# Optimization experiments

Hardware: AMD Instinct MI355X
Metric: run time of the kernel (lower is better)

The kernel has to match this reference:

```python
import jax, jax.numpy as jnp
import numpy as np
from jax import lax

SOS_TOKEN = 0
PAD_LEN = 30  # tokenizer.pad_len -> number of greedy decode steps


def _gru_cell(x, h, w_ih, w_hh, b_ih, b_hh):
    # PyTorch GRU cell math. x,h: [B,H]; w_*: [3H,H]; b_*: [3H]
    gi = x @ w_ih.T + b_ih
    gh = h @ w_hh.T + b_hh
    i_r, i_z, i_n = jnp.split(gi, 3, axis=-1)
    h_r, h_z, h_n = jnp.split(gh, 3, axis=-1)
    r = jax.nn.sigmoid(i_r + h_r)
    z = jax.nn.sigmoid(i_z + h_z)
    n = jnp.tanh(i_n + r * h_n)
    return (1.0 - z) * n + z * h


def _sm_encode(sm_hidden, conv_w, conv_b, enc_w, enc_b):
    # sm_hidden: [B, L, C] -> conv over time with C input channels
    x = jnp.transpose(sm_hidden, (0, 2, 1))  # [B, C, L]
    conv = lax.conv_general_dilated(
        x, conv_w, window_strides=(1,), padding='VALID',
        dimension_numbers=('NCH', 'OIH', 'NCH'))  # [B, O, L-k+1]
    conv = jax.nn.relu(conv + conv_b[None, :, None])
    pooled = jnp.max(conv, axis=-1)  # [B, O]
    return jax.nn.relu(pooled @ enc_w.T + enc_b)  # [B, H]


def reference(sm_hidden, embedding, w_ih, w_hh, b_ih, b_hh,
              w_out, b_out, conv_w, conv_b, enc_w, enc_b):
    B = sm_hidden.shape[0]
    h0 = _sm_encode(sm_hidden, conv_w, conv_b, enc_w, enc_b)  # [B, H]

    # The original re-runs the GRU over the whole (append-only) prefix each
    # iteration; since the GRU is deterministic this equals incremental
    # single-step updates, which we do here.
    def step(carry, _):
        h, tok = carry
        emb = embedding[tok]                      # [B, H]
        h_new = _gru_cell(emb, h, w_ih, w_hh, b_ih, b_hh)
        logits = h_new @ w_out.T + b_out          # [B, V]
        tok_new = jnp.argmax(logits, axis=-1)     # greedy topk(1)
        return (h_new, tok_new), (h_new, tok_new)

    tok0 = jnp.full((B,), SOS_TOKEN, dtype=jnp.int32)
    (h_last, _), (hiddens, toks) = lax.scan(step, (h0, tok0), None, length=PAD_LEN)

    decoder_output = jax.nn.log_softmax(h_last @ w_out.T + b_out, axis=1)  # [B, V]
    decoder_hidden = hiddens  # [PAD_LEN, B, H] == rnn_out of final _base_forward
    decoded_indices = jnp.concatenate([tok0[None, :], toks], axis=0)  # [PAD_LEN+1, B]
    return decoder_output, decoder_hidden, decoded_indices


def setup_inputs() -> dict:
    key = jax.random.key(0)
    ks = jax.random.split(key, 12)
    B, L, C = 512, 120, 128
    H, V, O, K = 1024, 512, 32, 10
    s = 1.0 / np.sqrt(H)
    return {
        'sm_hidden': jax.random.normal(ks[0], (B, L, C), jnp.float32),
        'embedding': jax.random.normal(ks[1], (V, H), jnp.float32),
        'w_ih': jax.random.uniform(ks[2], (3 * H, H), jnp.float32, -s, s),
        'w_hh': jax.random.uniform(ks[3], (3 * H, H), jnp.float32, -s, s),
        'b_ih': jax.random.uniform(ks[4], (3 * H,), jnp.float32, -s, s),
        'b_hh': jax.random.uniform(ks[5], (3 * H,), jnp.float32, -s, s),
        'w_out': jax.random.uniform(ks[6], (V, H), jnp.float32, -s, s),
        'b_out': jax.random.uniform(ks[7], (V,), jnp.float32, -s, s),
        'conv_w': jax.random.normal(ks[8], (O, C, K), jnp.float32) * 0.05,
        'conv_b': jax.random.normal(ks[9], (O,), jnp.float32) * 0.05,
        'enc_w': jax.random.uniform(ks[10], (H, O), jnp.float32, -s, s),
        'enc_b': jax.random.uniform(ks[11], (H,), jnp.float32, -s, s),
    }
```

## Files before the change

kernel.cpp:

```cpp
#include <hip/hip_runtime.h>
#include <hip/hip_bf16.h>
#include <math.h>

#define Bsz 512
#define Hd 1024
#define Vd 512
#define Cc 128
#define Ll 120
#define Kk 10
#define Oo 32
#define NSTEP 30

typedef __attribute__((ext_vector_type(8))) short bf16x8;
typedef __attribute__((ext_vector_type(4))) float f32x4;
typedef unsigned short ushort;
typedef unsigned long long u64;

#define BARLDS() asm volatile("s_waitcnt lgkmcnt(0)\n\ts_barrier" ::: "memory")

static __device__ __forceinline__ float sigm(float x) { return 1.f / (1.f + expf(-x)); }
static __device__ __forceinline__ ushort f2bf(float x) {
    __hip_bfloat16 h = __float2bfloat16(x);
    return *(ushort*)&h;
}
static __device__ __forceinline__ float bf2f(ushort u) {
    __hip_bfloat16 h; *(ushort*)&h = u;
    return __bfloat162float(h);
}
static __device__ __forceinline__ unsigned monofy(float f) {
    unsigned u = __float_as_uint(f);
    return (u & 0x80000000u) ? ~u : (u | 0x80000000u);
}

__global__ void k_packall(const float* __restrict__ wih, ushort* __restrict__ wihH, ushort* __restrict__ wihL,
                          const float* __restrict__ whh, ushort* __restrict__ whhH, ushort* __restrict__ whhL,
                          const float* __restrict__ wout, ushort* __restrict__ woutH, ushort* __restrict__ woutL,
                          const float* __restrict__ emb, ushort* __restrict__ embH, ushort* __restrict__ embL) {
    int gidx = blockIdx.x * 256 + threadIdx.x;
    const float* W;
    ushort *hi, *lo;
    int idx;
    if (gidx < 3145728)      { W = wih;  hi = wihH;  lo = wihL;  idx = gidx; }
    else if (gidx < 6291456) { W = whh;  hi = whhH;  lo = whhL;  idx = gidx - 3145728; }
    else if (gidx < 6815744) { W = wout; hi = woutH; lo = woutL; idx = gidx - 6291456; }
    else if (gidx < 7340032) { W = emb;  hi = embH;  lo = embL;  idx = gidx - 6815744; }
    else return;
    int jj = idx & 7, l = (idx >> 3) & 63, c = (idx >> 9) & 31, nf = idx >> 14;
    int n = nf * 16 + (l & 15);
    int k = c * 32 + ((l >> 4) << 3) + jj;
    float v = W[(size_t)n * 1024 + k];
    ushort h = f2bf(v);
    hi[idx] = h;
    lo[idx] = f2bf(v - bf2f(h));
}

__global__ void k_packconv(const float* __restrict__ cw, ushort* __restrict__ hi,
                           ushort* __restrict__ lo) {
    int idx = blockIdx.x * 256 + threadIdx.x;
    if (idx >= 2 * 40 * 64 * 8) return;
    int jj = idx & 7, l = (idx >> 3) & 63, ch = (idx >> 9) % 40, nf = idx / (40 * 512);
    int o = nf * 16 + (l & 15);
    int k = ch * 32 + ((l >> 4) << 3) + jj;
    int kc = k >> 7, c = k & 127;
    float v = cw[(o * Cc + c) * Kk + kc];
    ushort h = f2bf(v);
    hi[idx] = h;
    lo[idx] = f2bf(v - bf2f(h));
}

__global__ __launch_bounds__(512) void k_convmfma(const float* __restrict__ sm,
                                                  const ushort* __restrict__ wH,
                                                  const ushort* __restrict__ wL,
                                                  const float* __restrict__ cb,
                                                  const float* __restrict__ ew,
                                                  const float* __restrict__ eb,
                                                  float* __restrict__ h0,
                                                  ushort* __restrict__ ApHi,
                                                  ushort* __restrict__ ApLo) {
    __shared__ ushort hiS[2][137 * 128];
    __shared__ ushort loS[2][137 * 128];
    __shared__ float sred[8][2][2][16];
    __shared__ float ps[2][Oo];
    int b0 = blockIdx.x * 2, tid = threadIdx.x, wid = tid >> 6, l = tid & 63;

    for (int i = tid; i < 3840; i += 512) {
        int s = i >= 1920;
        int local = i - s * 1920;
        int row = local >> 4, col0 = (local & 15) * 8;
        const float* smb = sm + (size_t)(b0 + s) * (Ll * Cc);
        float4 fa = *(const float4*)(smb + row * Cc + col0);
        float4 fb = *(const float4*)(smb + row * Cc + col0 + 4);
        float vv[8] = {fa.x, fa.y, fa.z, fa.w, fb.x, fb.y, fb.z, fb.w};
        ushort h8[8], l8[8];
#pragma unroll
        for (int q = 0; q < 8; ++q) {
            ushort h = f2bf(vv[q]);
            h8[q] = h;
            l8[q] = f2bf(vv[q] - bf2f(h));
        }
        int o = ((row << 8) + (col0 << 1)) ^ ((row & 7) << 4);
        *(bf16x8*)((char*)hiS[s] + o) = *(bf16x8*)h8;
        *(bf16x8*)((char*)loS[s] + o) = *(bf16x8*)l8;
    }
    __syncthreads();

    f32x4 acc[2][2];
#pragma unroll
    for (int s = 0; s < 2; ++s)
#pragma unroll
        for (int j = 0; j < 2; ++j) acc[s][j] = (f32x4)0.f;

    bf16x8 aH0[2], aL0[2], bH0[2], bL0[2];
    bf16x8 aH1[2], aL1[2], bH1[2], bL1[2];

#define CLD(AH, AL, BH, BL, ch)                                                        \
    {                                                                                  \
        int row = wid * 16 + (l & 15) + ((ch) >> 2);                                   \
        int o = ((row << 8) + ((((ch) & 3) * 32 + ((l >> 4) << 3)) << 1))              \
                ^ ((row & 7) << 4);                                                    \
        _Pragma("unroll") for (int s = 0; s < 2; ++s) {                                \
            AH[s] = *(const bf16x8*)((const char*)hiS[s] + o);                         \
            AL[s] = *(const bf16x8*)((const char*)loS[s] + o);                         \
        }                                                                              \
        _Pragma("unroll") for (int nf = 0; nf < 2; ++nf) {                             \
            int boff = ((nf * 40 + (ch)) * 64 + l) * 8;                                \
            BH[nf] = *(const bf16x8*)(wH + boff);                                      \
            BL[nf] = *(const bf16x8*)(wL + boff);                                      \
        }                                                                              \
    }
#define CST(AH, AL, BH, BL)                                                            \
    {                                                                                  \
        _Pragma("unroll") for (int s = 0; s < 2; ++s)                                  \
            _Pragma("unroll") for (int nf = 0; nf < 2; ++nf) {                         \
                acc[s][nf] = __builtin_amdgcn_mfma_f32_16x16x32_bf16(AH[s], BH[nf], acc[s][nf], 0, 0, 0); \
                acc[s][nf] = __builtin_amdgcn_mfma_f32_16x16x32_bf16(AH[s], BL[nf], acc[s][nf], 0, 0, 0); \
                acc[s][nf] = __builtin_amdgcn_mfma_f32_16x16x32_bf16(AL[s], BH[nf], acc[s][nf], 0, 0, 0); \
            }                                                                          \
    }

    CLD(aH0, aL0, bH0, bL0, 0)
#pragma unroll
    for (int ch = 0; ch < 40; ch += 2) {
        CLD(aH1, aL1, bH1, bL1, ch + 1)
        CST(aH0, aL0, bH0, bL0)
        if (ch + 2 < 40) CLD(aH0, aL0, bH0, bL0, ch + 2)
        CST(aH1, aL1, bH1, bL1)
    }
#undef CLD
#undef CST

    float mx[2][2] = {{-1e38f, -1e38f}, {-1e38f, -1e38f}};
    {
        int tb = wid * 16 + ((l >> 4) << 2);
#pragma unroll
        for (int q = 0; q < 4; ++q) {
            if (tb + q <= 110) {
#pragma unroll
                for (int s = 0; s < 2; ++s) {
                    mx[s][0] = fmaxf(mx[s][0], acc[s][0][q]);
                    mx[s][1] = fmaxf(mx[s][1], acc[s][1][q]);
                }
            }
        }
    }
#pragma unroll
    for (int sh = 16; sh < 64; sh <<= 1) {
#pragma unroll
        for (int s = 0; s < 2; ++s) {
            mx[s][0] = fmaxf(mx[s][0], __shfl_xor(mx[s][0], sh));
            mx[s][1] = fmaxf(mx[s][1], __shfl_xor(mx[s][1], sh));
        }
    }
    if (l < 16) {
#pragma unroll
        for (int s = 0; s < 2; ++s) {
            sred[wid][s][0][l] = mx[s][0];
            sred[wid][s][1][l] = mx[s][1];
        }
    }
    __syncthreads();
    if (tid < 64) {
        int s = tid >> 5, o = tid & 31;
        float m = sred[0][s][o >> 4][o & 15];
#pragma unroll
        for (int w = 1; w < 8; ++w) m = fmaxf(m, sred[w][s][o >> 4][o & 15]);
        ps[s][o] = fmaxf(m + cb[o], 0.f);
    }
    __syncthreads();
    for (int j = tid; j < Hd; j += 512) {
        const float4* e4 = (const float4*)(ew + (size_t)j * Oo);
        float4 w0 = e4[0], w1 = e4[1], w2 = e4[2], w3 = e4[3];
        float4 w4 = e4[4], w5 = e4[5], w6 = e4[6], w7 = e4[7];
        float ebj = eb[j];
        int c = j >> 5, sub = (j >> 3) & 3, jj = j & 7;
#pragma unroll
        for (int s = 0; s < 2; ++s) {
            int b = b0 + s;
            const float* p = ps[s];
            float a = ebj;
            a += p[0] * w0.x + p[1] * w0.y + p[2] * w0.z + p[3] * w0.w;
            a += p[4] * w1.x + p[5] * w1.y + p[6] * w1.z + p[7] * w1.w;
            a += p[8] * w2.x + p[9] * w2.y + p[10] * w2.z + p[11] * w2.w;
            a += p[12] * w3.x + p[13] * w3.y + p[14] * w3.z + p[15] * w3.w;
            a += p[16] * w4.x + p[17] * w4.y + p[18] * w4.z + p[19] * w4.w;
            a += p[20] * w5.x + p[21] * w5.y + p[22] * w5.z + p[23] * w5.w;
            a += p[24] * w6.x + p[25] * w6.y + p[26] * w6.z + p[27] * w6.w;
            a += p[28] * w7.x + p[29] * w7.y + p[30] * w7.z + p[31] * w7.w;
            a = fmaxf(a, 0.f);
            h0[(size_t)b * Hd + j] = a;
            ushort hb = f2bf(a);
            ushort lb = f2bf(a - bf2f(hb));
            int amf = b >> 4;
            int lane_r = (b & 15) + (sub << 4);
            int flat = ((amf * 32 + c) * 64 + lane_r) * 8 + jj;
            ApHi[flat] = hb;
            ApLo[flat] = lb;
        }
    }
}

template <int EPI>
__global__ __launch_bounds__(512, 2) void k_rnn(const ushort* __restrict__ Ah,
                                                const ushort* __restrict__ Al,
                                                const ushort* __restrict__ Bh,
                                                const ushort* __restrict__ Bl,
                                                const float* __restrict__ bias,
                                                float* __restrict__ outF,
                                                const float* __restrict__ gi_all,
                                                const u64* __restrict__ pkRd,
                                                u64* __restrict__ pkWr,
                                                float* __restrict__ outIdxRow,
                                                const float* __restrict__ hOld,
                                                ushort* __restrict__ ApHi,
                                                ushort* __restrict__ ApLo) {
    __shared__ ushort Bs[2][48][512];
    int id = blockIdx.x;
    int xcd = id & 7, r = id >> 3;
    int jt = xcd * 4 + (r & 3);
    int mt = r >> 2;
    int tid = threadIdx.x, wid = tid >> 6, l = tid & 63;
    int wm = wid >> 1, wj = wid & 1;
    int mf = mt * 4 + wm;
    int jf = jt * 2 + wj;
    int jcol = jf * 16 + (l & 15);

    float giR[4][3], hR[4];
    int bR[4], tkR[4];
    if constexpr (EPI == 1) {
#pragma unroll
        for (int q = 0; q < 4; ++q) {
            bR[q] = mf * 16 + ((l >> 4) << 2) + q;
            u64 pk = pkRd[bR[q]];
            tkR[q] = 511 - (int)(unsigned)(pk & 0xFFFFFFFFu);
            const float* gi = gi_all + (size_t)tkR[q] * 3072;
            giR[q][0] = gi[jcol];
            giR[q][1] = gi[1024 + jcol];
            giR[q][2] = gi[2048 + jcol];
            hR[q] = hOld[(size_t)bR[q] * 1024 + jcol];
        }
        if (jt == 0 && wj == 0 && (l & 15) == 0) {
#pragma unroll
            for (int q = 0; q < 4; ++q) {
                pkWr[bR[q]] = 0ULL;
                if (outIdxRow) outIdxRow[bR[q]] = (float)tkR[q];
            }
        }
    }

    f32x4 acc[3];
#pragma unroll
    for (int g = 0; g < 3; ++g) acc[g] = (f32x4)0.f;

    bf16x8 stg[6], aH0[4], aL0[4], aH1[4], aL1[4];

#define STG_LD(it)                                                                     \
    {                                                                                  \
        _Pragma("unroll") for (int k = 0; k < 6; ++k) {                                \
            int u = wid + 8 * k;                                                       \
            int hl = u & 1, wjb = (u >> 1) & 1, g = (u >> 2) % 3, cu = u / 12;         \
            const ushort* sp = hl ? Bl : Bh;                                           \
            stg[k] = *(const bf16x8*)(sp +                                             \
                (size_t)(((g * 64 + jt * 2 + wjb) * 32 + (it) * 4 + cu) * 64 + l) * 8);\
        }                                                                              \
    }
#define STG_WR(buf)                                                                    \
    {                                                                                  \
        _Pragma("unroll") for (int k = 0; k < 6; ++k)                                  \
            *(bf16x8*)&Bs[buf][wid + 8 * k][l * 8] = stg[k];                           \
    }
#define A_LD(DH, DL, it)                                                               \
    {                                                                                  \
        _Pragma("unroll") for (int cc = 0; cc < 4; ++cc) {                             \
            DH[cc] = *(const bf16x8*)(Ah + (size_t)((mf * 32 + (it) * 4 + cc) * 64 + l) * 8); \
            DL[cc] = *(const bf16x8*)(Al + (size_t)((mf * 32 + (it) * 4 + cc) * 64 + l) * 8); \
        }                                                                              \
    }
#define CMP(buf, AH, AL)                                                               \
    {                                                                                  \
        _Pragma("unroll") for (int cc = 0; cc < 4; ++cc)                               \
            _Pragma("unroll") for (int g = 0; g < 3; ++g) {                            \
                bf16x8 bhh = *(const bf16x8*)&Bs[buf][cc * 12 + g * 4 + wj * 2 + 0][l * 8]; \
                bf16x8 bll = *(const bf16x8*)&Bs[buf][cc * 12 + g * 4 + wj * 2 + 1][l * 8]; \
                acc[g] = __builtin_amdgcn_mfma_f32_16x16x32_bf16(AH[cc], bhh, acc[g], 0, 0, 0); \
                acc[g] = __builtin_amdgcn_mfma_f32_16x16x32_bf16(AH[cc], bll, acc[g], 0, 0, 0); \
                acc[g] = __builtin_amdgcn_mfma_f32_16x16x32_bf16(AL[cc], bhh, acc[g], 0, 0, 0); \
            }                                                                          \
    }

    STG_LD(0)
    STG_WR(0)
    STG_LD(1)
    A_LD(aH0, aL0, 0)
    BARLDS();
#pragma unroll
    for (int it = 0; it < 8; ++it) {
        int buf = it & 1;
        if (it < 7) STG_WR(buf ^ 1)
        if (it < 6) STG_LD(it + 2)
        if (it & 1) {
            if (it < 7) A_LD(aH0, aL0, it + 1)
            CMP(buf, aH1, aL1)
        } else {
            if (it < 7) A_LD(aH1, aL1, it + 1)
            CMP(buf, aH0, aL0)
        }
        BARLDS();
    }
#undef STG_LD
#undef STG_WR
#undef A_LD
#undef CMP

    if constexpr (EPI == 0) {
#pragma unroll
        for (int q = 0; q < 4; ++q) {
            int b = mf * 16 + ((l >> 4) << 2) + q;
#pragma unroll
            for (int g = 0; g < 3; ++g)
                outF[(size_t)b * 3072 + g * 1024 + jcol] =
                    acc[g][q] + bias[g * 1024 + jcol];
        }
    } else {
        float bj0 = bias[jcol], bj1 = bias[1024 + jcol], bj2 = bias[2048 + jcol];
        int c = jcol >> 5, sub = (jcol >> 3) & 3, jj = jcol & 7;
#pragma unroll
        for (int q = 0; q < 4; ++q) {
            int b = bR[q];
            float rr = sigm(giR[q][0] + acc[0][q] + bj0);
            float zz = sigm(giR[q][1] + acc[1][q] + bj1);
            float nn = tanhf(giR[q][2] + rr * (acc[2][q] + bj2));
            float hv = (1.f - zz) * nn + zz * hR[q];
            outF[(size_t)b * 1024 + jcol] = hv;
            ushort hb = f2bf(hv);
            ushort lb = f2bf(hv - bf2f(hb));
            int lane_r = (b & 15) + (sub << 4);
            int flat = (((b >> 4) * 32 + c) * 64 + lane_r) * 8 + jj;
            ApHi[flat] = hb;
            ApLo[flat] = lb;
        }
    }
}

__global__ __launch_bounds__(256) void k_lgt(const ushort* __restrict__ Ah,
                                             const ushort* __restrict__ Al,
                                             const ushort* __restrict__ Bh,
                                             const ushort* __restrict__ Bl,
                                             const float* __restrict__ bias,
                                             float* __restrict__ outF,
                                             u64* __restrict__ pkOut) {
    __shared__ ushort Bs[2][8][512];
    int id = blockIdx.x;
    int xcd = id & 7, r = id >> 3;
    int vf = xcd * 4 + (r & 3);
    int mg = r >> 2;
    int tid = threadIdx.x, w = tid >> 6, l = tid & 63;
    int mf = mg * 4 + w;

    f32x4 acc = (f32x4)0.f;
    bf16x8 stg[2];
    bf16x8 a0h[4], a0l[4], a1h[4], a1l[4];

#define LSTG_LD(it)                                                                    \
    {                                                                                  \
        _Pragma("unroll") for (int k = 0; k < 2; ++k) {                                \
            int s = tid + 256 * k;                                                     \
            int il = s & 63, u = s >> 6;                                               \
            int hl = u & 1, cu = u >> 1;                                               \
            const ushort* sp = hl ? Bl : Bh;                                           \
            stg[k] = *(const bf16x8*)(sp +                                             \
                (size_t)((vf * 32 + (it) * 4 + cu) * 64 + il) * 8);                    \
        }                                                                              \
    }
#define LSTG_WR(buf)                                                                   \
    {                                                                                  \
        _Pragma("unroll") for (int k = 0; k < 2; ++k) {                                \
            int s = tid + 256 * k;                                                     \
            int il = s & 63, u = s >> 6;                                               \
            *(bf16x8*)&Bs[buf][u][il * 8] = stg[k];                                    \
        }                                                                              \
    }
#define LA_LD(DH, DL, it)                                                              \
    {                                                                                  \
        _Pragma("unroll") for (int cu = 0; cu < 4; ++cu) {                             \
            size_t aoff = (size_t)((mf * 32 + (it) * 4 + cu) * 64 + l) * 8;            \
            DH[cu] = *(const bf16x8*)(Ah + aoff);                                      \
            DL[cu] = *(const bf16x8*)(Al + aoff);                                      \
        }                                                                              \
    }
#define LCMP(buf, AH, AL)                                                              \
    {                                                                                  \
        _Pragma("unroll") for (int cu = 0; cu < 4; ++cu) {                             \
            bf16x8 bh = *(const bf16x8*)&Bs[buf][cu * 2 + 0][l * 8];                   \
            bf16x8 bl = *(const bf16x8*)&Bs[buf][cu * 2 + 1][l * 8];                   \
            acc = __builtin_amdgcn_mfma_f32_16x16x32_bf16(AH[cu], bh, acc, 0, 0, 0);   \
            acc = __builtin_amdgcn_mfma_f32_16x16x32_bf16(AH[cu], bl, acc, 0, 0, 0);   \
            acc = __builtin_amdgcn_mfma_f32_16x16x32_bf16(AL[cu], bh, acc, 0, 0, 0);   \
        }                                                                              \
    }

    LSTG_LD(0)
    LSTG_WR(0)
    LSTG_LD(1)
    LA_LD(a0h, a0l, 0)
    BARLDS();
#pragma unroll
    for (int it = 0; it < 8; ++it) {
        int buf = it & 1;
        if (it < 7) LSTG_WR(buf ^ 1)
        if (it < 6) LSTG_LD(it + 2)
        if (it & 1) {
            if (it < 7) LA_LD(a0h, a0l, it + 1)
            LCMP(buf, a1h, a1l)
        } else {
            if (it < 7) LA_LD(a1h, a1l, it + 1)
            LCMP(buf, a0h, a0l)
        }
        BARLDS();
    }
#undef LSTG_LD
#undef LSTG_WR
#undef LA_LD
#undef LCMP

    int v = vf * 16 + (l & 15);
    float bv = bias[v];
    float lg[4];
    unsigned vmq[4];
#pragma unroll
    for (int q = 0; q < 4; ++q) {
        int b = mf * 16 + ((l >> 4) << 2) + q;
        lg[q] = acc[q] + bv;
        if (outF) outF[(size_t)b * Vd + v] = lg[q];
        vmq[q] = 511u - (unsigned)v;
    }
#pragma unroll
    for (int off = 1; off < 16; off <<= 1) {
#pragma unroll
        for (int q = 0; q < 4; ++q) {
            float og = __shfl_xor(lg[q], off);
            unsigned ov = __shfl_xor(vmq[q], off);
            if (og > lg[q] || (og == lg[q] && ov > vmq[q])) { lg[q] = og; vmq[q] = ov; }
        }
    }
    if ((l & 15) == 0) {
#pragma unroll
        for (int q = 0; q < 4; ++q) {
            int b = mf * 16 + ((l >> 4) << 2) + q;
            u64 pk = ((u64)monofy(lg[q]) << 32) | (u64)vmq[q];
            atomicMax(&pkOut[b], pk);
        }
    }
}

__global__ __launch_bounds__(64) void k_fin(const float* __restrict__ logits,
                                            const u64* __restrict__ pk,
                                            float* __restrict__ out_lsm,
                                            float* __restrict__ outIdxRow) {
    int b = blockIdx.x, l = threadIdx.x;
    const float* row = logits + (size_t)b * Vd;
    float bv = -3.4e38f;
#pragma unroll
    for (int s = 0; s < 8; ++s) bv = fmaxf(bv, row[s * 64 + l]);
#pragma unroll
    for (int off = 1; off < 64; off <<= 1) bv = fmaxf(bv, __shfl_xor(bv, off));
    float sum = 0.f;
#pragma unroll
    for (int s = 0; s < 8; ++s) sum += expf(row[s * 64 + l] - bv);
#pragma unroll
    for (int off = 1; off < 64; off <<= 1) sum += __shfl_xor(sum, off);
    float lse = logf(sum) + bv;
#pragma unroll
    for (int s = 0; s < 8; ++s) {
        int v = s * 64 + l;
        out_lsm[(size_t)b * Vd + v] = row[v] - lse;
    }
    if (l == 0)
        outIdxRow[b] = (float)(511 - (int)(unsigned)(pk[b] & 0xFFFFFFFFu));
}

__global__ void k_init(u64* __restrict__ P0, float* __restrict__ out_idx0) {
    int i = blockIdx.x * 64 + threadIdx.x;
    if (i < Bsz) {
        P0[i] = (1ULL << 32) | 511ULL;
        out_idx0[i] = 0.f;
    }
}

extern "C" void kernel_launch(void* const* d_in, const int* in_sizes, int n_in,
                              void* d_out, int out_size, void* d_ws, size_t ws_size,
                              hipStream_t stream) {
    const float* sm    = (const float*)d_in[0];
    const float* emb   = (const float*)d_in[1];
    const float* w_ih  = (const float*)d_in[2];
    const float* w_hh  = (const float*)d_in[3];
    const float* b_ih  = (const float*)d_in[4];
    const float* b_hh  = (const float*)d_in[5];
    const float* w_out = (const float*)d_in[6];
    const float* b_out = (const float*)d_in[7];
    const float* cw    = (const float*)d_in[8];
    const float* cb    = (const float*)d_in[9];
    const float* ew    = (const float*)d_in[10];
    const float* eb    = (const float*)d_in[11];

    float* out0 = (float*)d_out;
    float* out1 = out0 + (size_t)Bsz * Vd;
    float* out2 = out1 + (size_t)NSTEP * Bsz * Hd;

    char* wsp = (char*)d_ws;
    float*  f_gi  = (float*)wsp;  wsp += sizeof(float) * Bsz * 3072;
    float*  f_h0  = (float*)wsp;  wsp += sizeof(float) * Bsz * Hd;
    float*  f_log = (float*)wsp;  wsp += sizeof(float) * Bsz * Vd;
    u64*    Ppk0  = (u64*)wsp;    wsp += sizeof(u64) * Bsz;
    u64*    Ppk1  = (u64*)wsp;    wsp += sizeof(u64) * Bsz;
    ushort* ApHi0 = (ushort*)wsp; wsp += sizeof(ushort) * Bsz * Hd;
    ushort* ApLo0 = (ushort*)wsp; wsp += sizeof(ushort) * Bsz * Hd;
    ushort* ApHi1 = (ushort*)wsp; wsp += sizeof(ushort) * Bsz * Hd;
    ushort* ApLo1 = (ushort*)wsp; wsp += sizeof(ushort) * Bsz * Hd;
    ushort* embH  = (ushort*)wsp; wsp += sizeof(ushort) * Vd * Hd;
    ushort* embL  = (ushort*)wsp; wsp += sizeof(ushort) * Vd * Hd;
    ushort* wihH  = (ushort*)wsp; wsp += sizeof(ushort) * 3072 * Hd;
    ushort* wihL  = (ushort*)wsp; wsp += sizeof(ushort) * 3072 * Hd;
    ushort* whhH  = (ushort*)wsp; wsp += sizeof(ushort) * 3072 * Hd;
    ushort* whhL  = (ushort*)wsp; wsp += sizeof(ushort) * 3072 * Hd;
    ushort* woutH = (ushort*)wsp; wsp += sizeof(ushort) * Vd * Hd;
    ushort* woutL = (ushort*)wsp; wsp += sizeof(ushort) * Vd * Hd;
    ushort* cwBH  = (ushort*)wsp; wsp += sizeof(ushort) * 2 * 40 * 64 * 8;
    ushort* cwBL  = (ushort*)wsp; wsp += sizeof(ushort) * 2 * 40 * 64 * 8;

    k_packconv<<<160, 256, 0, stream>>>(cw, cwBH, cwBL);
    k_packall<<<(7340032 + 255) / 256, 256, 0, stream>>>(
        w_ih, wihH, wihL, w_hh, whhH, whhL, w_out, woutH, woutL, emb, embH, embL);
    k_convmfma<<<256, 512, 0, stream>>>(sm, cwBH, cwBL, cb, ew, eb,
                                        f_h0, ApHi0, ApLo0);
    k_rnn<0><<<256, 512, 0, stream>>>(embH, embL, wihH, wihL, b_ih, f_gi,
                                      nullptr, nullptr, nullptr, nullptr, nullptr,
                                      nullptr, nullptr);
    k_init<<<8, 64, 0, stream>>>(Ppk0, out2);

    ushort* aH[2] = {ApHi0, ApHi1};
    ushort* aL[2] = {ApLo0, ApLo1};
    u64* P[2] = {Ppk0, Ppk1};
    for (int t = 0; t < NSTEP; ++t) {
        int cur = t & 1, nxt = cur ^ 1;
        const float* hOld = (t == 0) ? f_h0 : (out1 + (size_t)(t - 1) * Bsz * Hd);
        k_rnn<1><<<256, 512, 0, stream>>>(
            aH[cur], aL[cur], whhH, whhL, b_hh, out1 + (size_t)t * Bsz * Hd,
            f_gi, P[cur], P[nxt],
            (t >= 1) ? (out2 + (size_t)t * Bsz) : nullptr,
            hOld, aH[nxt], aL[nxt]);
        k_lgt<<<256, 256, 0, stream>>>(aH[nxt], aL[nxt], woutH, woutL, b_out,
                                       (t == NSTEP - 1) ? f_log : nullptr,
                                       P[nxt]);
    }
    k_fin<<<Bsz, 64, 0, stream>>>(f_log, P[NSTEP & 1], out0,
                                  out2 + (size_t)NSTEP * Bsz);
}
```

Measured before the change: 764.2 us.

## Split recurrent GRU kernel into smaller-tile variant with more blocks

```diff
diff --git a/kernel.cpp b/kernel.cpp
--- a/kernel.cpp
+++ b/kernel.cpp
@@ -219,20 +219,12 @@
     }
 }
 
-template <int EPI>
-__global__ __launch_bounds__(512, 2) void k_rnn(const ushort* __restrict__ Ah,
-                                                const ushort* __restrict__ Al,
-                                                const ushort* __restrict__ Bh,
-                                                const ushort* __restrict__ Bl,
-                                                const float* __restrict__ bias,
-                                                float* __restrict__ outF,
-                                                const float* __restrict__ gi_all,
-                                                const u64* __restrict__ pkRd,
-                                                u64* __restrict__ pkWr,
-                                                float* __restrict__ outIdxRow,
-                                                const float* __restrict__ hOld,
-                                                ushort* __restrict__ ApHi,
-                                                ushort* __restrict__ ApLo) {
+__global__ __launch_bounds__(512, 2) void k_gi(const ushort* __restrict__ Ah,
+                                               const ushort* __restrict__ Al,
+                                               const ushort* __restrict__ Bh,
+                                               const ushort* __restrict__ Bl,
+                                               const float* __restrict__ bias,
+                                               float* __restrict__ outF) {
     __shared__ ushort Bs[2][48][512];
     int id = blockIdx.x;
     int xcd = id & 7, r = id >> 3;
@@ -244,29 +236,6 @@
     int jf = jt * 2 + wj;
     int jcol = jf * 16 + (l & 15);
 
-    float giR[4][3], hR[4];
-    int bR[4], tkR[4];
-    if constexpr (EPI == 1) {
-#pragma unroll
-        for (int q = 0; q < 4; ++q) {
-            bR[q] = mf * 16 + ((l >> 4) << 2) + q;
-            u64 pk = pkRd[bR[q]];
-            tkR[q] = 511 - (int)(unsigned)(pk & 0xFFFFFFFFu);
-            const float* gi = gi_all + (size_t)tkR[q] * 3072;
-            giR[q][0] = gi[jcol];
-            giR[q][1] = gi[1024 + jcol];
-            giR[q][2] = gi[2048 + jcol];
-            hR[q] = hOld[(size_t)bR[q] * 1024 + jcol];
-        }
-        if (jt == 0 && wj == 0 && (l & 15) == 0) {
-#pragma unroll
-            for (int q = 0; q < 4; ++q) {
-                pkWr[bR[q]] = 0ULL;
-                if (outIdxRow) outIdxRow[bR[q]] = (float)tkR[q];
-            }
-        }
-    }
-
     f32x4 acc[3];
 #pragma unroll
     for (int g = 0; g < 3; ++g) acc[g] = (f32x4)0.f;
@@ -331,16 +300,129 @@
 #undef A_LD
 #undef CMP
 
-    if constexpr (EPI == 0) {
+#pragma unroll
+    for (int q = 0; q < 4; ++q) {
+        int b = mf * 16 + ((l >> 4) << 2) + q;
+#pragma unroll
+        for (int g = 0; g < 3; ++g)
+            outF[(size_t)b * 3072 + g * 1024 + jcol] = acc[g][q] + bias[g * 1024 + jcol];
+    }
+}
+
+__global__ __launch_bounds__(256, 2) void k_rnnS(const ushort* __restrict__ Ah,
+                                                 const ushort* __restrict__ Al,
+                                                 const ushort* __restrict__ Bh,
+                                                 const ushort* __restrict__ Bl,
+                                                 const float* __restrict__ bias,
+                                                 float* __restrict__ outF,
+                                                 const float* __restrict__ gi_all,
+                                                 const u64* __restrict__ pkRd,
+                                                 u64* __restrict__ pkWr,
+                                                 float* __restrict__ outIdxRow,
+                                                 const float* __restrict__ hOld,
+                                                 ushort* __restrict__ ApHi,
+                                                 ushort* __restrict__ ApLo) {
+    __shared__ ushort Bs[2][12][512];
+    int id = blockIdx.x;
+    int xcd = id & 7, r = id >> 3;
+    int jf = xcd * 8 + (r & 7);
+    int mt = r >> 3;
+    int tid = threadIdx.x, wm = tid >> 6, l = tid & 63;
+    int mf = mt * 4 + wm;
+    int jcol = jf * 16 + (l & 15);
+
+    f32x4 acc[3];
+#pragma unroll
+    for (int g = 0; g < 3; ++g) acc[g] = (f32x4)0.f;
+
+    bf16x8 stg[3], aH0[2], aL0[2], aH1[2], aL1[2];
+
+#define SSTG_LD(it)                                                                    \
+    {                                                                                  \
+        _Pragma("unroll") for (int k = 0; k < 3; ++k) {                                \
+            int s = tid + 256 * k;                                                     \
+            int il = s & 63, u = s >> 6;                                               \
+            int hl = u & 1, g = (u >> 1) % 3, cu = u / 6;                              \
+            const ushort* sp = hl ? Bl : Bh;                                           \
+            stg[k] = *(const bf16x8*)(sp +                                             \
+                (size_t)(((g * 64 + jf) * 32 + (it) * 2 + cu) * 64 + il) * 8);         \
+        }                                                                              \
+    }
+#define SSTG_WR(buf)                                                                   \
+    {                                                                                  \
+        _Pragma("unroll") for (int k = 0; k < 3; ++k) {                                \
+            int s = tid + 256 * k;                                                     \
+            int il = s & 63, u = s >> 6;                                               \
+            *(bf16x8*)&Bs[buf][u][il * 8] = stg[k];                                    \
+        }                                                                              \
+    }
+#define SA_LD(DH, DL, it)                                                              \
+    {                                                                                  \
+        _Pragma("unroll") for (int cc = 0; cc < 2; ++cc) {                             \
+            size_t off = (size_t)((mf * 32 + (it) * 2 + cc) * 64 + l) * 8;             \
+            DH[cc] = *(const bf16x8*)(Ah + off);                                       \
+            DL[cc] = *(const bf16x8*)(Al + off);                                       \
+        }                                                                              \
+    }
+#define SCMP(buf, AH, AL)                                                              \
+    {                                                                                  \
+        _Pragma("unroll") for (int cc = 0; cc < 2; ++cc)                               \
+            _Pragma("unroll") for (int g = 0; g < 3; ++g) {                            \
+                bf16x8 bhh = *(const bf16x8*)&Bs[buf][cc * 6 + g * 2 + 0][l * 8];      \
+                bf16x8 bll = *(const bf16x8*)&Bs[buf][cc * 6 + g * 2 + 1][l * 8];      \
+                acc[g] = __builtin_amdgcn_mfma_f32_16x16x32_bf16(AH[cc], bhh, acc[g], 0, 0, 0); \
+                acc[g] = __builtin_amdgcn_mfma_f32_16x16x32_bf16(AH[cc], bll, acc[g], 0, 0, 0); \
+                acc[g] = __builtin_amdgcn_mfma_f32_16x16x32_bf16(AL[cc], bhh, acc[g], 0, 0, 0); \
+            }                                                                          \
+    }
+
+    SSTG_LD(0)
+    SSTG_WR(0)
+    SSTG_LD(1)
+    SA_LD(aH0, aL0, 0)
+
+    float giR[4][3], hR[4];
+    int bR[4], tkR[4];
+#pragma unroll
+    for (int q = 0; q < 4; ++q) {
+        bR[q] = mf * 16 + ((l >> 4) << 2) + q;
+        u64 pk = pkRd[bR[q]];
+        tkR[q] = 511 - (int)(unsigned)(pk & 0xFFFFFFFFu);
+        const float* gi = gi_all + (size_t)tkR[q] * 3072;
+        giR[q][0] = gi[jcol];
+        giR[q][1] = gi[1024 + jcol];
+        giR[q][2] = gi[2048 + jcol];
+        hR[q] = hOld[(size_t)bR[q] * 1024 + jcol];
+    }
+    if (jf == 0 && (l & 15) == 0) {
 #pragma unroll
         for (int q = 0; q < 4; ++q) {
-            int b = mf * 16 + ((l >> 4) << 2) + q;
-#pragma unroll
-            for (int g = 0; g < 3; ++g)
-                outF[(size_t)b * 3072 + g * 1024 + jcol] =
-                    acc[g][q] + bias[g * 1024 + jcol];
-        }
-    } else {
+            pkWr[bR[q]] = 0ULL;
+            if (outIdxRow) outIdxRow[bR[q]] = (float)tkR[q];
+        }
+    }
+
+    BARLDS();
+#pragma unroll
+    for (int it = 0; it < 16; ++it) {
+        int buf = it & 1;
+        if (it < 15) SSTG_WR(buf ^ 1)
+        if (it < 14) SSTG_LD(it + 2)
+        if (it & 1) {
+            if (it < 15) SA_LD(aH0, aL0, it + 1)
+            SCMP(buf, aH1, aL1)
+        } else {
+            if (it < 15) SA_LD(aH1, aL1, it + 1)
+            SCMP(buf, aH0, aL0)
+        }
+        BARLDS();
+    }
+#undef SSTG_LD
+#undef SSTG_WR
+#undef SA_LD
+#undef SCMP
+
+    {
         float bj0 = bias[jcol], bj1 = bias[1024 + jcol], bj2 = bias[2048 + jcol];
         int c = jcol >> 5, sub = (jcol >> 3) & 3, jj = jcol & 7;
 #pragma unroll
@@ -552,9 +634,7 @@
         w_ih, wihH, wihL, w_hh, whhH, whhL, w_out, woutH, woutL, emb, embH, embL);
     k_convmfma<<<256, 512, 0, stream>>>(sm, cwBH, cwBL, cb, ew, eb,
                                         f_h0, ApHi0, ApLo0);
-    k_rnn<0><<<256, 512, 0, stream>>>(embH, embL, wihH, wihL, b_ih, f_gi,
-                                      nullptr, nullptr, nullptr, nullptr, nullptr,
-                                      nullptr, nullptr);
+    k_gi<<<256, 512, 0, stream>>>(embH, embL, wihH, wihL, b_ih, f_gi);
     k_init<<<8, 64, 0, stream>>>(Ppk0, out2);
 
     ushort* aH[2] = {ApHi0, ApHi1};
@@ -563,7 +643,7 @@
     for (int t = 0; t < NSTEP; ++t) {
         int cur = t & 1, nxt = cur ^ 1;
         const float* hOld = (t == 0) ? f_h0 : (out1 + (size_t)(t - 1) * Bsz * Hd);
-        k_rnn<1><<<256, 512, 0, stream>>>(
+        k_rnnS<<<512, 256, 0, stream>>>(
             aH[cur], aL[cur], whhH, whhL, b_hh, out1 + (size_t)t * Bsz * Hd,
             f_gi, P[cur], P[nxt],
             (t >= 1) ? (out2 + (size_t)t * Bsz) : nullptr,
```

Result: no change. 751.8 us (median of 2 runs) (-1.6%).
